# Kernel tuning notes

Hardware: AMD Instinct MI355X
Metric: run time of the kernel (lower is better)

## Reference

```python
import jax, jax.numpy as jnp
import numpy as np

NUM_HEADS = 8
B, L, D = 4, 1024, 512


def sinusoidal_embeddings(length, dim, decay_term=10000.0):
    positions = jnp.arange(1 - length, length, dtype=jnp.float32).reshape(-1, 1)
    div_term = jnp.exp(-jnp.arange(0, dim, 2, dtype=jnp.float32) * (np.log(decay_term) / dim))
    return jnp.concatenate([jnp.sin(positions * div_term), jnp.cos(positions * div_term)], axis=1)


def setup_inputs() -> dict:
    key = jax.random.key(0)
    k1, k2 = jax.random.split(key)
    x = jax.random.normal(k1, (B, L, D), dtype=jnp.float32)
    W = jax.random.normal(k2, (D, 3 * D), dtype=jnp.float32) * 0.02
    b = jnp.zeros((3 * D,), dtype=jnp.float32)
    return {"x": x, "W": W, "b": b}


def reference(x, W, b):
    batch, length, dim = x.shape
    d_head = dim // NUM_HEADS
    # pointwise Conv(3*dim, kernel_size=1) == dense projection
    proj = jnp.einsum('bld,de->ble', x, W) + b  # [B, L, 3*dim]
    # split heads exactly as the module: reshape to [B,L,H,3*d_head], move heads, split into q,k,v
    proj = proj.reshape(batch, length, NUM_HEADS, 3 * d_head).transpose(0, 2, 1, 3)
    q, k, v = jnp.split(proj, 3, axis=3)  # each [B, H, L, d_head]
    qk = jnp.einsum('bhqd,bhkd->bhqk', q, k)
    # relative position scores via gather (unoptimized path)
    emb_matrix = sinusoidal_embeddings(length, d_head)  # [2L-1, d_head]
    indices = jnp.arange(length)[:, None] - jnp.arange(length) + length - 1  # [L, L]
    embeddings = emb_matrix[indices]  # [L, L, d_head]
    qe = jnp.einsum('bhqd,qkd->bhqk', q, embeddings)
    weights = jax.nn.softmax((qk + qe) / jnp.sqrt(jnp.float32(d_head)), axis=-1)
    output = jnp.einsum('bhqk,bhkd->bhqd', weights, v)
    return output.transpose(0, 2, 1, 3).reshape(batch, length, dim)
```

## Files before the change

### kernel.cpp

```cpp
#include <hip/hip_runtime.h>

typedef unsigned short UST;
typedef __attribute__((ext_vector_type(8))) __bf16 bf16x8;
typedef __attribute__((ext_vector_type(4))) float f32x4;
typedef __attribute__((ext_vector_type(16))) float f32x16;

#define NB 4
#define NH 8
#define LSEQ 1024
#define DMODEL 512
#define DH 64

__device__ __forceinline__ UST f2bf(float f) {
  union { float f; unsigned u; } v; v.f = f;
  unsigned u = v.u;
  return (UST)((u + 0x7FFFu + ((u >> 16) & 1u)) >> 16);
}
__device__ __forceinline__ float bf2f(UST h) {
  union { unsigned u; float f; } v; v.u = ((unsigned)h) << 16;
  return v.f;
}
__device__ __forceinline__ unsigned cvt_pk_bf16(float lo, float hi) {
  unsigned r;
  asm volatile("v_cvt_pk_bf16_f32 %0, %1, %2" : "=v"(r) : "v"(lo), "v"(hi));
  return r;
}

__global__ void k_convert_x(const float* __restrict__ x, UST* __restrict__ xbf) {
  int i = blockIdx.x * 256 + threadIdx.x;
  float4 v = ((const float4*)x)[i];
  ushort4 o;
  o.x = f2bf(v.x); o.y = f2bf(v.y); o.z = f2bf(v.z); o.w = f2bf(v.w);
  ((ushort4*)xbf)[i] = o;
}

__global__ void k_transpose_W(const float* __restrict__ W, UST* __restrict__ WT) {
  __shared__ float tile[64][65];
  int n0 = blockIdx.x * 64;
  int k0 = blockIdx.y * 64;
  int tx = threadIdx.x & 63, ty = threadIdx.x >> 6;
#pragma unroll
  for (int i = 0; i < 16; ++i) {
    int k = ty + i * 4;
    tile[k][tx] = W[(size_t)(k0 + k) * 1536 + n0 + tx];
  }
  __syncthreads();
#pragma unroll
  for (int i = 0; i < 16; ++i) {
    int n = ty + i * 4;
    WT[(size_t)(n0 + n) * 512 + k0 + tx] = f2bf(tile[tx][n]);
  }
}

__global__ __launch_bounds__(256) void k_proj(
    const UST* __restrict__ xbf, const UST* __restrict__ WT, const float* __restrict__ bias,
    UST* __restrict__ qext, UST* __restrict__ kext, UST* __restrict__ vT) {
  int m0 = blockIdx.x * 128;
  int n0 = blockIdx.y * 64;
  int t = threadIdx.x;
  int lane = t & 63, w = t >> 6;
  int wr = w >> 1, wc = w & 1;
  int g = lane >> 4, c16 = lane & 15;

  __shared__ UST AtS[128 * 64];
  __shared__ UST BtS[64 * 64];

  const char* Ag = (const char*)(xbf + (size_t)m0 * 512);
  const char* Bg = (const char*)(WT + (size_t)n0 * 512);

  bf16x8 areg[4], breg[2];
#pragma unroll
  for (int c = 0; c < 4; ++c) {
    int u = c * 256 + t, r = u >> 3, s = u & 7;
    areg[c] = *(const bf16x8*)(Ag + (size_t)r * 1024 + s * 16);
  }
#pragma unroll
  for (int c = 0; c < 2; ++c) {
    int u = c * 256 + t, r = u >> 3, s = u & 7;
    breg[c] = *(const bf16x8*)(Bg + (size_t)r * 1024 + s * 16);
  }

  f32x4 acc[4][2] = {};
  for (int kk = 0; kk < 512; kk += 64) {
    __syncthreads();
#pragma unroll
    for (int c = 0; c < 4; ++c) {
      int u = c * 256 + t, r = u >> 3, s = u & 7;
      *(bf16x8*)((char*)AtS + (size_t)r * 128 + (s ^ (r & 7)) * 16) = areg[c];
    }
#pragma unroll
    for (int c = 0; c < 2; ++c) {
      int u = c * 256 + t, r = u >> 3, s = u & 7;
      *(bf16x8*)((char*)BtS + (size_t)r * 128 + (s ^ (r & 7)) * 16) = breg[c];
    }
    __syncthreads();

    if (kk + 64 < 512) {
      size_t cb = (size_t)(kk + 64) * 2;
#pragma unroll
      for (int c = 0; c < 4; ++c) {
        int u = c * 256 + t, r = u >> 3, s = u & 7;
        areg[c] = *(const bf16x8*)(Ag + (size_t)r * 1024 + cb + s * 16);
      }
#pragma unroll
      for (int c = 0; c < 2; ++c) {
        int u = c * 256 + t, r = u >> 3, s = u & 7;
        breg[c] = *(const bf16x8*)(Bg + (size_t)r * 1024 + cb + s * 16);
      }
    }

#pragma unroll
    for (int kf = 0; kf < 2; ++kf) {
      bf16x8 af[4], bfr[2];
#pragma unroll
      for (int rf = 0; rf < 4; ++rf) {
        int r = wr * 64 + rf * 16 + c16;
        int s = (kf * 4 + g) ^ (r & 7);
        af[rf] = *(const bf16x8*)((const char*)AtS + (size_t)r * 128 + s * 16);
      }
#pragma unroll
      for (int cf = 0; cf < 2; ++cf) {
        int r = wc * 32 + cf * 16 + c16;
        int s = (kf * 4 + g) ^ (r & 7);
        bfr[cf] = *(const bf16x8*)((const char*)BtS + (size_t)r * 128 + s * 16);
      }
      __builtin_amdgcn_s_setprio(1);
#pragma unroll
      for (int rf = 0; rf < 4; ++rf)
#pragma unroll
        for (int cf = 0; cf < 2; ++cf)
          acc[rf][cf] = __builtin_amdgcn_mfma_f32_16x16x32_bf16(af[rf], bfr[cf], acc[rf][cf], 0, 0, 0);
      __builtin_amdgcn_s_setprio(0);
    }
  }

#pragma unroll
  for (int rf = 0; rf < 4; ++rf) {
#pragma unroll
    for (int cf = 0; cf < 2; ++cf) {
      int c = n0 + wc * 32 + cf * 16 + c16;
      int h = c / 192, rem = c % 192;
      float bv = bias[c];
#pragma unroll
      for (int r = 0; r < 4; ++r) {
        int row = m0 + wr * 64 + rf * 16 + g * 4 + r;
        int bidx = row >> 10, ltok = row & 1023;
        int bh = bidx * 8 + h;
        float val = acc[rf][cf][r] + bv;
        if (rem < 64)
          qext[((size_t)bh * 1024 + ltok) * 128 + rem] = f2bf(val * 0.125f);
        else if (rem < 128)
          kext[((size_t)bh * 1024 + ltok) * 128 + (rem - 64)] = f2bf(val);
        else
          vT[((size_t)bh * 64 + (rem - 128)) * 1024 + ltok] = f2bf(val);
      }
    }
  }
}

__global__ void k_relpos(UST* __restrict__ qext, UST* __restrict__ kext) {
  int gid = blockIdx.x * 256 + threadIdx.x;
  int j = gid & 31;
  int l = (gid >> 5) & 1023;
  int bh = gid >> 15;
  float dd = exp2f((float)(-2 * j) * 0.20762050593046f);
  float ang = (float)l * dd;
  float s = __sinf(ang), c = __cosf(ang);
  UST* qp = qext + ((size_t)bh * 1024 + l) * 128;
  float qs = bf2f(qp[j]), qc = bf2f(qp[32 + j]);
  qp[64 + j] = f2bf(qs * s + qc * c);
  qp[96 + j] = f2bf(qc * s - qs * c);
  UST* kp = kext + ((size_t)bh * 1024 + l) * 128;
  kp[64 + j] = f2bf(c);
  kp[96 + j] = f2bf(s);
}

__global__ __launch_bounds__(256) void k_attn(
    const UST* __restrict__ qext, const UST* __restrict__ kext,
    const UST* __restrict__ vT, float* __restrict__ out) {
  int blk = ((blockIdx.x & 7) << 6) | (blockIdx.x >> 3);
  int qt = blk & 15, bh = blk >> 4;
  int b = bh >> 3, h = bh & 7;
  int q0 = qt * 64;
  int t = threadIdx.x;
  int lane = t & 63, w = t >> 6;
  int l31 = lane & 31, lh = lane >> 5;
  int wq = w >> 1, wk = w & 1;

  __shared__ UST KtS[2][64 * 128];
  __shared__ UST VtS[2][64 * 64];
  __shared__ float Lsum[2][2][32];

  const UST* qbase = qext + ((size_t)bh * 1024 + q0 + wq * 32 + l31) * 128 + lh * 8;
  bf16x8 qf[8];
#pragma unroll
  for (int c = 0; c < 8; ++c) qf[c] = *(const bf16x8*)&qbase[c * 16];

  const char* kgbase = (const char*)(kext + (size_t)bh * 1024 * 128);
  const char* vgbase = (const char*)(vT + (size_t)bh * 64 * 1024);

  f32x16 O[2] = {};
  float l_lane = 0.f;

  bf16x8 kreg[4], vreg[2];
#pragma unroll
  for (int c = 0; c < 4; ++c) {
    int u = c * 256 + t;
    kreg[c] = *(const bf16x8*)(kgbase + (size_t)(u >> 4) * 256 + (u & 15) * 16);
  }
#pragma unroll
  for (int c = 0; c < 2; ++c) {
    int u = c * 256 + t;
    vreg[c] = *(const bf16x8*)(vgbase + (size_t)(u >> 3) * 2048 + (u & 7) * 16);
  }
#pragma unroll
  for (int c = 0; c < 4; ++c) {
    int u = c * 256 + t, r = u >> 4, s = u & 15;
    *(bf16x8*)((char*)KtS[0] + (size_t)r * 256 + (s ^ ((r ^ (r >> 3)) & 7)) * 16) = kreg[c];
  }
#pragma unroll
  for (int c = 0; c < 2; ++c) {
    int u = c * 256 + t, r = u >> 3, s = u & 7;
    *(bf16x8*)((char*)VtS[0] + (size_t)r * 128 + (s ^ ((r ^ (r >> 3)) & 7)) * 16) = vreg[c];
  }
#pragma unroll
  for (int c = 0; c < 4; ++c) {
    int u = c * 256 + t;
    kreg[c] = *(const bf16x8*)(kgbase + 64 * 256 + (size_t)(u >> 4) * 256 + (u & 15) * 16);
  }
#pragma unroll
  for (int c = 0; c < 2; ++c) {
    int u = c * 256 + t;
    vreg[c] = *(const bf16x8*)(vgbase + 64 * 2 + (size_t)(u >> 3) * 2048 + (u & 7) * 16);
  }
  __syncthreads();

  int krow = wk * 32 + l31;
  int ksalt = (krow ^ (krow >> 3)) & 7;

  for (int it = 0; it < 16; ++it) {
    int cur = it & 1;
    const char* Kb = (const char*)(KtS[cur]);
    const char* Vb = (const char*)(VtS[cur]);

    f32x16 sa = {};
#pragma unroll
    for (int kh = 0; kh < 2; ++kh) {
      bf16x8 kfr[4];
#pragma unroll
      for (int kc = 0; kc < 4; ++kc) {
        int slot = ((kh * 4 + kc) * 2 + lh) ^ ksalt;
        kfr[kc] = *(const bf16x8*)(Kb + (size_t)krow * 256 + slot * 16);
      }
      __builtin_amdgcn_s_setprio(1);
#pragma unroll
      for (int kc = 0; kc < 4; ++kc)
        sa = __builtin_amdgcn_mfma_f32_32x32x16_bf16(kfr[kc], qf[kh * 4 + kc], sa, 0, 0, 0);
      __builtin_amdgcn_s_setprio(0);
    }

    float p[16];
#pragma unroll
    for (int i = 0; i < 16; ++i) {
      p[i] = __expf(sa[i]);
      l_lane += p[i];
    }
    unsigned wv[8], xv[8];
#pragma unroll
    for (int j = 0; j < 8; ++j) wv[j] = cvt_pk_bf16(p[2 * j], p[2 * j + 1]);
#pragma unroll
    for (int j = 0; j < 8; ++j) xv[j] = (unsigned)__shfl_xor((int)wv[j], 32, 64);
    int4 pa0i = lh ? (int4){(int)xv[2], (int)xv[3], (int)wv[2], (int)wv[3]}
                   : (int4){(int)wv[0], (int)wv[1], (int)xv[0], (int)xv[1]};
    int4 pa1i = lh ? (int4){(int)xv[6], (int)xv[7], (int)wv[6], (int)wv[7]}
                   : (int4){(int)wv[4], (int)wv[5], (int)xv[4], (int)xv[5]};
    bf16x8 pa[2] = {*(bf16x8*)&pa0i, *(bf16x8*)&pa1i};

#pragma unroll
    for (int dn = 0; dn < 2; ++dn) {
      int d = dn * 32 + l31;
      int dsalt = (d ^ (d >> 3)) & 7;
      bf16x8 vf[2];
#pragma unroll
      for (int kc = 0; kc < 2; ++kc) {
        int slot = (wk * 4 + kc * 2 + lh) ^ dsalt;
        vf[kc] = *(const bf16x8*)(Vb + (size_t)d * 128 + slot * 16);
      }
      __builtin_amdgcn_s_setprio(1);
#pragma unroll
      for (int kc = 0; kc < 2; ++kc)
        O[dn] = __builtin_amdgcn_mfma_f32_32x32x16_bf16(pa[kc], vf[kc], O[dn], 0, 0, 0);
      __builtin_amdgcn_s_setprio(0);
    }

    if (it < 15) {
      char* Kw = (char*)(KtS[cur ^ 1]);
      char* Vw = (char*)(VtS[cur ^ 1]);
#pragma unroll
      for (int c = 0; c < 4; ++c) {
        int u = c * 256 + t, r = u >> 4, s = u & 15;
        *(bf16x8*)(Kw + (size_t)r * 256 + (s ^ ((r ^ (r >> 3)) & 7)) * 16) = kreg[c];
      }
#pragma unroll
      for (int c = 0; c < 2; ++c) {
        int u = c * 256 + t, r = u >> 3, s = u & 7;
        *(bf16x8*)(Vw + (size_t)r * 128 + (s ^ ((r ^ (r >> 3)) & 7)) * 16) = vreg[c];
      }
      if (it < 14) {
        const char* kg = kgbase + (size_t)(it + 2) * 64 * 256;
#pragma unroll
        for (int c = 0; c < 4; ++c) {
          int u = c * 256 + t;
          kreg[c] = *(const bf16x8*)(kg + (size_t)(u >> 4) * 256 + (u & 15) * 16);
        }
        const char* vg = vgbase + (size_t)(it + 2) * 64 * 2;
#pragma unroll
        for (int c = 0; c < 2; ++c) {
          int u = c * 256 + t;
          vreg[c] = *(const bf16x8*)(vg + (size_t)(u >> 3) * 2048 + (u & 7) * 16);
        }
      }
    }
    __syncthreads();
  }

  l_lane += __shfl_xor(l_lane, 32, 64);
  if (lh == 0) Lsum[wk][wq][l31] = l_lane;
  float* scratch = (float*)KtS[0];
  if (wk == 1) {
#pragma unroll
    for (int i = 0; i < 16; ++i) {
      int qr = wq * 32 + ((i & 3) + 8 * (i >> 2) + 4 * lh);
      scratch[qr * 64 + l31] = O[0][i];
      scratch[qr * 64 + 32 + l31] = O[1][i];
    }
  }
  __syncthreads();
  if (wk == 0) {
#pragma unroll
    for (int i = 0; i < 16; ++i) {
      int cr = (i & 3) + 8 * (i >> 2) + 4 * lh;
      int qr = wq * 32 + cr;
      float inv = 1.0f / (Lsum[0][wq][cr] + Lsum[1][wq][cr]);
      float* op = out + ((size_t)b * 1024 + q0 + qr) * 512 + h * 64;
      op[l31] = (O[0][i] + scratch[qr * 64 + l31]) * inv;
      op[32 + l31] = (O[1][i] + scratch[qr * 64 + 32 + l31]) * inv;
    }
  }
}

extern "C" void kernel_launch(void* const* d_in, const int* in_sizes, int n_in,
                              void* d_out, int out_size, void* d_ws, size_t ws_size,
                              hipStream_t stream) {
  const float* x = (const float*)d_in[0];
  const float* W = (const float*)d_in[1];
  const float* bias = (const float*)d_in[2];
  float* out = (float*)d_out;

  UST* ws = (UST*)d_ws;
  UST* xbf  = ws;
  UST* WT   = xbf + 4096 * 512;
  UST* qext = WT + 1536 * 512;
  UST* kext = qext + 32 * 1024 * 128;
  UST* vT   = kext + 32 * 1024 * 128;

  k_convert_x<<<dim3(2048), dim3(256), 0, stream>>>(x, xbf);
  k_transpose_W<<<dim3(24, 8), dim3(256), 0, stream>>>(W, WT);
  k_proj<<<dim3(32, 24), dim3(256), 0, stream>>>(xbf, WT, bias, qext, kext, vT);
  k_relpos<<<dim3(4096), dim3(256), 0, stream>>>(qext, kext);
  k_attn<<<dim3(512), dim3(256), 0, stream>>>(qext, kext, vT, out);
}
```

Before: 58.05 us.

## Fuse relative-position kernel into conversion and projection epilogue

Removes the separate k_relpos launch. The constant sin/cos part of kext is now written by extra blocks in the x-conversion kernel. The q-dependent rotated components are computed in the projection epilogue from q values staged in shared memory. This saves one kernel launch and a global re-read of q. In exchange, one third of projection blocks take an extra barrier and some serial transcendental work in the epilogue.

```diff
diff --git a/kernel.cpp b/kernel.cpp
--- a/kernel.cpp
+++ b/kernel.cpp
@@ -26,12 +26,27 @@
   return r;
 }
 
-__global__ void k_convert_x(const float* __restrict__ x, UST* __restrict__ xbf) {
-  int i = blockIdx.x * 256 + threadIdx.x;
-  float4 v = ((const float4*)x)[i];
-  ushort4 o;
-  o.x = f2bf(v.x); o.y = f2bf(v.y); o.z = f2bf(v.z); o.w = f2bf(v.w);
-  ((ushort4*)xbf)[i] = o;
+__global__ void k_convert_x(const float* __restrict__ x, UST* __restrict__ xbf,
+                            UST* __restrict__ kext) {
+  int bid = blockIdx.x;
+  if (bid < 2048) {
+    int i = bid * 256 + threadIdx.x;
+    float4 v = ((const float4*)x)[i];
+    ushort4 o;
+    o.x = f2bf(v.x); o.y = f2bf(v.y); o.z = f2bf(v.z); o.w = f2bf(v.w);
+    ((ushort4*)xbf)[i] = o;
+  } else {
+    int gid = (bid - 2048) * 256 + threadIdx.x;
+    int j = gid & 31;
+    int l = (gid >> 5) & 1023;
+    int bh = gid >> 15;
+    float dd = exp2f((float)(-2 * j) * 0.20762050593046f);
+    float ang = (float)l * dd;
+    float s = __sinf(ang), c = __cosf(ang);
+    UST* kp = kext + ((size_t)bh * 1024 + l) * 128;
+    kp[64 + j] = f2bf(c);
+    kp[96 + j] = f2bf(s);
+  }
 }
 
 __global__ void k_transpose_W(const float* __restrict__ W, UST* __restrict__ WT) {
@@ -134,6 +149,9 @@
     }
   }
 
+  bool doalpha = (blockIdx.y % 3 == 0);
+  if (doalpha) __syncthreads();
+
 #pragma unroll
   for (int rf = 0; rf < 4; ++rf) {
 #pragma unroll
@@ -147,32 +165,39 @@
         int bidx = row >> 10, ltok = row & 1023;
         int bh = bidx * 8 + h;
         float val = acc[rf][cf][r] + bv;
-        if (rem < 64)
-          qext[((size_t)bh * 1024 + ltok) * 128 + rem] = f2bf(val * 0.125f);
-        else if (rem < 128)
+        if (rem < 64) {
+          UST qv = f2bf(val * 0.125f);
+          qext[((size_t)bh * 1024 + ltok) * 128 + rem] = qv;
+          if (doalpha)
+            AtS[(size_t)(row - m0) * 64 + rem] = qv;
+        } else if (rem < 128)
           kext[((size_t)bh * 1024 + ltok) * 128 + (rem - 64)] = f2bf(val);
         else
           vT[((size_t)bh * 64 + (rem - 128)) * 1024 + ltok] = f2bf(val);
       }
     }
   }
-}
-
-__global__ void k_relpos(UST* __restrict__ qext, UST* __restrict__ kext) {
-  int gid = blockIdx.x * 256 + threadIdx.x;
-  int j = gid & 31;
-  int l = (gid >> 5) & 1023;
-  int bh = gid >> 15;
-  float dd = exp2f((float)(-2 * j) * 0.20762050593046f);
-  float ang = (float)l * dd;
-  float s = __sinf(ang), c = __cosf(ang);
-  UST* qp = qext + ((size_t)bh * 1024 + l) * 128;
-  float qs = bf2f(qp[j]), qc = bf2f(qp[32 + j]);
-  qp[64 + j] = f2bf(qs * s + qc * c);
-  qp[96 + j] = f2bf(qc * s - qs * c);
-  UST* kp = kext + ((size_t)bh * 1024 + l) * 128;
-  kp[64 + j] = f2bf(c);
-  kp[96 + j] = f2bf(s);
+
+  if (doalpha) {
+    __syncthreads();
+    int hh = blockIdx.y / 3;
+    int rr = t >> 1;
+    int row = m0 + rr;
+    int bidx = row >> 10, ltok = row & 1023;
+    int bh = bidx * 8 + hh;
+    UST* qp = qext + ((size_t)bh * 1024 + ltok) * 128;
+#pragma unroll
+    for (int i = 0; i < 16; ++i) {
+      int j = (t & 1) * 16 + i;
+      float dd = exp2f((float)(-2 * j) * 0.20762050593046f);
+      float ang = (float)ltok * dd;
+      float s = __sinf(ang), c = __cosf(ang);
+      float qs = bf2f(AtS[(size_t)rr * 64 + j]);
+      float qc = bf2f(AtS[(size_t)rr * 64 + 32 + j]);
+      qp[64 + j] = f2bf(qs * s + qc * c);
+      qp[96 + j] = f2bf(qc * s - qs * c);
+    }
+  }
 }
 
 __global__ __launch_bounds__(256) void k_attn(
@@ -364,9 +389,8 @@
   UST* kext = qext + 32 * 1024 * 128;
   UST* vT   = kext + 32 * 1024 * 128;
 
-  k_convert_x<<<dim3(2048), dim3(256), 0, stream>>>(x, xbf);
+  k_convert_x<<<dim3(6144), dim3(256), 0, stream>>>(x, xbf, kext);
   k_transpose_W<<<dim3(24, 8), dim3(256), 0, stream>>>(W, WT);
   k_proj<<<dim3(32, 24), dim3(256), 0, stream>>>(xbf, WT, bias, qext, kext, vT);
-  k_relpos<<<dim3(4096), dim3(256), 0, stream>>>(qext, kext);
   k_attn<<<dim3(512), dim3(256), 0, stream>>>(qext, kext, vT, out);
 }
```

Measured after the change: 56.61 us. -2.5%, faster.
